# Kernel optimization log

Measured on AMD Instinct MI355X. Metric: run time of the kernel, lower is better.

The kernel has to match this reference:

```python
import jax, jax.numpy as jnp
import numpy as np

V_IN = 40962
V_POOL = 10242  # (V_IN + 6) // 4, icosahedral mesh
EPS = 1e-5


def _bn(x, g, b):
    # x: (B, V, C); per-sample BatchNorm1d over vertex axis (track_running_stats=False)
    m = jnp.mean(x, axis=1, keepdims=True)
    v = jnp.mean((x - m) ** 2, axis=1, keepdims=True)  # biased variance, as torch BN
    return (x - m) * jax.lax.rsqrt(v + EPS) * g + b


def _conv(x, idx, W, b):
    # x: (B, V, C); idx: (7*V,) neighbor order indices -> (B, V, 7*C) @ W + b
    B, V, C = x.shape
    g = x[:, idx, :].reshape(B, V, 7 * C)
    return jnp.einsum('bvk,ko->bvo', g, W) + b


def _lrelu(x):
    return jnp.where(x >= 0, x, 0.2 * x)


def setup_inputs() -> dict:
    key = jax.random.key(0)
    ks = jax.random.split(key, 4)
    C_in, C_out = 64, 128
    x = jax.random.normal(ks[0], (16, C_in, V_IN), dtype=jnp.float32)
    pool_neigh_orders = jax.random.randint(ks[1], (7 * V_POOL,), 0, V_IN, dtype=jnp.int64)
    neigh_orders = jax.random.randint(ks[2], (7 * V_POOL,), 0, V_POOL, dtype=jnp.int64)
    kw1, kw2 = jax.random.split(ks[3])
    W1 = jax.random.normal(kw1, (7 * C_in, C_out), dtype=jnp.float32) * 0.05
    W2 = jax.random.normal(kw2, (7 * C_out, C_out), dtype=jnp.float32) * 0.05
    return {
        'x': x,
        'pool_neigh_orders': pool_neigh_orders,
        'neigh_orders': neigh_orders,
        'W1': W1, 'b1': jnp.zeros((C_out,), jnp.float32),
        'g1': jnp.ones((C_out,), jnp.float32), 'beta1': jnp.zeros((C_out,), jnp.float32),
        'W2': W2, 'b2': jnp.zeros((C_out,), jnp.float32),
        'g2': jnp.ones((C_out,), jnp.float32), 'beta2': jnp.zeros((C_out,), jnp.float32),
    }


def reference(x, pool_neigh_orders, neigh_orders, W1, b1, g1, beta1, W2, b2, g2, beta2):
    # x: (B, C, V) -> work in (B, V, C)
    h = jnp.transpose(x, (0, 2, 1))
    B, _, C = h.shape
    # mean pool: (B, V_POOL, 7, C).mean over neighbors
    h = h[:, pool_neigh_orders, :].reshape(B, V_POOL, 7, C).mean(axis=2)
    h = _lrelu(_bn(_conv(h, neigh_orders, W1, b1), g1, beta1))
    h = _lrelu(_bn(_conv(h, neigh_orders, W2, b2), g2, beta2))
    return jnp.transpose(h, (0, 2, 1))  # (B, out_ch, V_POOL)
```

## Files before the change

kernel.cpp:

```cpp
#include <hip/hip_runtime.h>
#include <hip/hip_bf16.h>

#define NB 16
#define VIN 40962
#define VP 10242
#define EPSbn 1e-5f

typedef __attribute__((ext_vector_type(8))) short bf16x8;
typedef __attribute__((ext_vector_type(4))) float f32x4;
typedef unsigned short u16;

static constexpr size_t OFF_W2 = 0;
static constexpr size_t OFF_W1 = 458752;
static constexpr size_t OFF_Y1 = 688128;
static constexpr size_t OFF_ST = OFF_Y1 + (size_t)NB * VP * 128 * 4;
static constexpr size_t WS_NEED = OFF_ST + 8 * (size_t)NB * 128 * 4;
static constexpr size_t OFF_XT = WS_NEED;
static constexpr size_t WS_FAST = OFF_XT + (size_t)NB * VIN * 64 * 4;

__device__ __forceinline__ u16 f2bf(float f) {
    unsigned u; __builtin_memcpy(&u, &f, 4);
    u = u + 0x7FFF + ((u >> 16) & 1);
    return (u16)(u >> 16);
}
__device__ __forceinline__ float bf2f(u16 h) {
    unsigned u = ((unsigned)h) << 16; float f; __builtin_memcpy(&f, &u, 4); return f;
}
__device__ __forceinline__ ushort2 splitf(float f) {
    u16 h = f2bf(f);
    u16 l = f2bf(f - bf2f(h));
    ushort2 r; r.x = h; r.y = l; return r;
}

__global__ void k_wsplit(const float* __restrict__ W, u16* __restrict__ wts, int K)
{
    int idx = blockIdx.x * 256 + threadIdx.x;
    if (idx >= K * 128) return;
    int k = idx >> 7, o = idx & 127;
    ushort2 s = splitf(W[idx]);
    wts[(size_t)o * 2 * K + k]     = s.x;
    wts[(size_t)o * 2 * K + K + k] = s.y;
}

__global__ void k_transpose(const float* __restrict__ x, float* __restrict__ xT)
{
    __shared__ float t[64][65];
    const int b   = blockIdx.y;
    const int v0  = blockIdx.x * 64;
    const int tid = threadIdx.x;
    const int lc  = tid & 63;
    const int lw  = tid >> 6;
    const float* xb = x + (size_t)b * 64 * VIN;
#pragma unroll
    for (int u = 0; u < 16; ++u) {
        const int c = lw * 16 + u;
        const int v = v0 + lc;
        t[c][lc] = (v < VIN) ? xb[(size_t)c * VIN + v] : 0.f;
    }
    __syncthreads();
    float* xTb = xT + (size_t)b * VIN * 64;
#pragma unroll
    for (int u = 0; u < 16; ++u) {
        const int v = v0 + lw * 16 + u;
        if (v < VIN) xTb[(size_t)v * 64 + lc] = t[lc][lw * 16 + u];
    }
}

__global__ void k_pool_fast(const float* __restrict__ xT, const int* __restrict__ pidx,
                            u16* __restrict__ h0s)
{
    const int b  = blockIdx.y;
    const int vp = blockIdx.x * 4 + (threadIdx.x >> 6);
    const int c  = threadIdx.x & 63;
    if (vp >= VP) return;
    const float* xb = xT + (size_t)b * VIN * 64;
    float s = 0.f;
#pragma unroll
    for (int j = 0; j < 7; ++j) {
        const int id = pidx[vp * 7 + j];
        s += xb[(size_t)id * 64 + c];
    }
    s *= (1.f / 7.f);
    *(ushort2*)(h0s + ((size_t)b * VP + vp) * 128 + 2 * c) = splitf(s);
}

__global__ void k_pool_direct(const float* __restrict__ x, const int* __restrict__ pidx,
                              u16* __restrict__ h0s)
{
    const int b  = blockIdx.y;
    const int vp = blockIdx.x * 4 + (threadIdx.x >> 6);
    const int c  = threadIdx.x & 63;
    if (vp >= VP) return;
    const float* xb = x + (size_t)(b * 64) * VIN;
    float s = 0.f;
#pragma unroll
    for (int j = 0; j < 7; ++j) {
        const int id = pidx[vp * 7 + j];
        s += xb[(size_t)c * VIN + id];
    }
    s *= (1.f / 7.f);
    *(ushort2*)(h0s + ((size_t)b * VP + vp) * 128 + 2 * c) = splitf(s);
}

template<int CIN, bool TRANSOUT>
__global__ __launch_bounds__(256, 2)
void k_convm(const u16* __restrict__ src, const int* __restrict__ nidx,
             const u16* __restrict__ wts, const float* __restrict__ bias,
             float* __restrict__ y, float* __restrict__ gsum, float* __restrict__ gsq)
{
    constexpr int K = 7 * CIN;
    __shared__ float lt[TRANSOUT ? 128 : 1][129];

    const int tid = threadIdx.x;
    const int w   = tid >> 6;
    const int l   = tid & 63;
    const int lg  = l >> 4;
    const int lr  = l & 15;
    const int b   = blockIdx.y;
    const int vp0 = blockIdx.x * 128;
    const int r0  = vp0 + w * 32;

    const u16* srcb = src + (size_t)b * VP * (2 * CIN);
    const int vc0 = (r0 + lr      < VP) ? (r0 + lr)      : (VP - 1);
    const int vc1 = (r0 + 16 + lr < VP) ? (r0 + 16 + lr) : (VP - 1);

    const u16* bb[8];
#pragma unroll
    for (int ct = 0; ct < 8; ++ct) bb[ct] = wts + (size_t)(ct * 16 + lr) * (2 * K);

    f32x4 acc[2][8];
#pragma unroll
    for (int t = 0; t < 2; ++t)
#pragma unroll
        for (int ct = 0; ct < 8; ++ct) acc[t][ct] = (f32x4){0.f, 0.f, 0.f, 0.f};

    for (int j = 0; j < 7; ++j) {
        const int id0 = nidx[vc0 * 7 + j];
        const int id1 = nidx[vc1 * 7 + j];
        const u16* a0 = srcb + (size_t)id0 * (2 * CIN);
        const u16* a1 = srcb + (size_t)id1 * (2 * CIN);
#pragma unroll
        for (int ks = 0; ks < CIN / 32; ++ks) {
            const int ko = ks * 32 + lg * 8;
            bf16x8 p00 = *(const bf16x8*)(a0 + 2 * ko);
            bf16x8 p01 = *(const bf16x8*)(a0 + 2 * ko + 8);
            bf16x8 p10 = *(const bf16x8*)(a1 + 2 * ko);
            bf16x8 p11 = *(const bf16x8*)(a1 + 2 * ko + 8);
            bf16x8 ah0 = {p00[0], p00[2], p00[4], p00[6], p01[0], p01[2], p01[4], p01[6]};
            bf16x8 al0 = {p00[1], p00[3], p00[5], p00[7], p01[1], p01[3], p01[5], p01[7]};
            bf16x8 ah1 = {p10[0], p10[2], p10[4], p10[6], p11[0], p11[2], p11[4], p11[6]};
            bf16x8 al1 = {p10[1], p10[3], p10[5], p10[7], p11[1], p11[3], p11[5], p11[7]};
            const int kw = j * CIN + ko;
#pragma unroll
            for (int ct = 0; ct < 8; ++ct) {
                bf16x8 bh = *(const bf16x8*)(bb[ct] + kw);
                bf16x8 bl = *(const bf16x8*)(bb[ct] + kw + K);
                acc[0][ct] = __builtin_amdgcn_mfma_f32_16x16x32_bf16(ah0, bh, acc[0][ct], 0, 0, 0);
                acc[1][ct] = __builtin_amdgcn_mfma_f32_16x16x32_bf16(ah1, bh, acc[1][ct], 0, 0, 0);
                acc[0][ct] = __builtin_amdgcn_mfma_f32_16x16x32_bf16(al0, bh, acc[0][ct], 0, 0, 0);
                acc[1][ct] = __builtin_amdgcn_mfma_f32_16x16x32_bf16(al1, bh, acc[1][ct], 0, 0, 0);
                acc[0][ct] = __builtin_amdgcn_mfma_f32_16x16x32_bf16(ah0, bl, acc[0][ct], 0, 0, 0);
                acc[1][ct] = __builtin_amdgcn_mfma_f32_16x16x32_bf16(ah1, bl, acc[1][ct], 0, 0, 0);
            }
        }
    }

    float ssum[8], ssq[8];
#pragma unroll
    for (int ct = 0; ct < 8; ++ct) { ssum[ct] = 0.f; ssq[ct] = 0.f; }

#pragma unroll
    for (int ct = 0; ct < 8; ++ct) {
        const float bia = bias[ct * 16 + lr];
#pragma unroll
        for (int t = 0; t < 2; ++t) {
#pragma unroll
            for (int r = 0; r < 4; ++r) {
                const int row = r0 + t * 16 + lg * 4 + r;
                const float v = acc[t][ct][r] + bia;
                const bool ok = (row < VP);
                if constexpr (TRANSOUT) {
                    lt[w * 32 + t * 16 + lg * 4 + r][ct * 16 + lr] = v;
                } else {
                    if (ok) y[((size_t)b * VP + row) * 128 + ct * 16 + lr] = v;
                }
                if (ok) { ssum[ct] += v; ssq[ct] += v * v; }
            }
        }
    }
#pragma unroll
    for (int ct = 0; ct < 8; ++ct) {
        float s = ssum[ct], q = ssq[ct];
        s += __shfl_xor(s, 16, 64); s += __shfl_xor(s, 32, 64);
        q += __shfl_xor(q, 16, 64); q += __shfl_xor(q, 32, 64);
        if (l < 16) {
            atomicAdd(&gsum[b * 128 + ct * 16 + l], s);
            atomicAdd(&gsq [b * 128 + ct * 16 + l], q);
        }
    }
    if constexpr (TRANSOUT) {
        __syncthreads();
#pragma unroll
        for (int u = 0; u < 64; ++u) {
            const int idx = u * 256 + tid;
            const int ch = idx >> 7, vv = idx & 127;
            if (vp0 + vv < VP)
                y[((size_t)b * 128 + ch) * VP + vp0 + vv] = lt[vv][ch];
        }
    }
}

__global__ void k_finalize(const float* __restrict__ gsum, const float* __restrict__ gsq,
                           const float* __restrict__ gam, const float* __restrict__ bet,
                           float* __restrict__ scale, float* __restrict__ shift)
{
    const int i = blockIdx.x * 256 + threadIdx.x;
    if (i >= NB * 128) return;
    const int o = i & 127;
    const float m   = gsum[i] * (1.f / VP);
    const float var = gsq[i] * (1.f / VP) - m * m;
    const float sc  = gam[o] * rsqrtf(var + EPSbn);
    scale[i] = sc;
    shift[i] = fmaf(-m, sc, bet[o]);
}

__global__ void k_bn1(void* __restrict__ y1v, const float* __restrict__ sc1,
                      const float* __restrict__ sh1)
{
    const int b = blockIdx.y;
    float2* p = (float2*)y1v + (size_t)b * VP * 64;
    for (int e = blockIdx.x * 256 + threadIdx.x; e < VP * 64; e += gridDim.x * 256) {
        const int c = (e & 63) * 2;
        float2 f = p[e];
        const float2 sc = *(const float2*)(sc1 + b * 128 + c);
        const float2 sh = *(const float2*)(sh1 + b * 128 + c);
        float a0 = fmaf(f.x, sc.x, sh.x); a0 = (a0 >= 0.f) ? a0 : 0.2f * a0;
        float a1 = fmaf(f.y, sc.y, sh.y); a1 = (a1 >= 0.f) ? a1 : 0.2f * a1;
        const ushort2 s0 = splitf(a0), s1 = splitf(a1);
        ushort4 o; o.x = s0.x; o.y = s0.y; o.z = s1.x; o.w = s1.y;
        *(ushort4*)(p + e) = o;
    }
}

__global__ void k_bnout(float* __restrict__ out, const float* __restrict__ scale,
                        const float* __restrict__ shift)
{
    const int bo = blockIdx.x;
    const float sc = scale[bo], sh = shift[bo];
    float* p = out + (size_t)bo * VP;
    for (int v = threadIdx.x; v < VP; v += 256) {
        float xv = fmaf(p[v], sc, sh);
        p[v] = (xv >= 0.f) ? xv : 0.2f * xv;
    }
}

extern "C" void kernel_launch(void* const* d_in, const int* in_sizes, int n_in,
                              void* d_out, int out_size, void* d_ws, size_t ws_size,
                              hipStream_t stream)
{
    (void)in_sizes; (void)n_in; (void)out_size;
    const float* x   = (const float*)d_in[0];
    const int*   pidx= (const int*)d_in[1];
    const int*   nidx= (const int*)d_in[2];
    const float* W1  = (const float*)d_in[3];
    const float* b1  = (const float*)d_in[4];
    const float* g1  = (const float*)d_in[5];
    const float* be1 = (const float*)d_in[6];
    const float* W2  = (const float*)d_in[7];
    const float* b2  = (const float*)d_in[8];
    const float* g2  = (const float*)d_in[9];
    const float* be2 = (const float*)d_in[10];
    float* out = (float*)d_out;
    char*  ws  = (char*)d_ws;

    if (ws_size < WS_NEED) return;

    u16*   wts2 = (u16*)(ws + OFF_W2);
    u16*   wts1 = (u16*)(ws + OFF_W1);
    float* y1   = (float*)(ws + OFF_Y1);
    float* st   = (float*)(ws + OFF_ST);
    float* sum1 = st;          float* sq1 = st + 2048;
    float* sum2 = st + 4096;   float* sq2 = st + 6144;
    float* sc1  = st + 8192;   float* sh1 = st + 10240;
    float* sc2  = st + 12288;  float* sh2 = st + 14336;
    u16*   h0s  = (u16*)d_out;

    hipMemsetAsync(st, 0, 4 * 2048 * sizeof(float), stream);
    k_wsplit<<<224, 256, 0, stream>>>(W1, wts1, 448);
    k_wsplit<<<448, 256, 0, stream>>>(W2, wts2, 896);

    dim3 gpool((VP + 3) / 4, NB);
    if (ws_size >= WS_FAST) {
        float* xT = (float*)(ws + OFF_XT);
        dim3 gt((VIN + 63) / 64, NB);
        k_transpose<<<gt, 256, 0, stream>>>(x, xT);
        k_pool_fast<<<gpool, 256, 0, stream>>>(xT, pidx, h0s);
    } else {
        k_pool_direct<<<gpool, 256, 0, stream>>>(x, pidx, h0s);
    }

    dim3 gconv((VP + 127) / 128, NB);
    k_convm<64, false><<<gconv, 256, 0, stream>>>(h0s, nidx, wts1, b1, y1, sum1, sq1);
    k_finalize<<<8, 256, 0, stream>>>(sum1, sq1, g1, be1, sc1, sh1);
    k_bn1<<<dim3(160, NB), 256, 0, stream>>>(y1, sc1, sh1);
    k_convm<128, true><<<gconv, 256, 0, stream>>>((const u16*)y1, nidx, wts2, b2, out, sum2, sq2);
    k_finalize<<<8, 256, 0, stream>>>(sum2, sq2, g2, be2, sc2, sh2);
    k_bnout<<<2048, 256, 0, stream>>>(out, sc2, sh2);
}
```

Before: 1.033 ms.

## Pre-swizzle weights and activations for direct MFMA loads, remap grid per XCD

Weights are written in an MFMA-fragment-tiled layout, and activations store their hi and lo bf16 planes in separate halves of each row. Each lane can then load ready-made bf16x8 operands without shuffling elements. The conv kernel drops the LDS transpose and writes float4 columns directly, hoists the neighbor indices into registers, and raises the occupancy target to 4. Blocks are remapped so each XCD handles two batches, aiming at better L2 locality. The higher occupancy bound may force register spilling, and the grid mapping hardcodes 81 tiles and 8 XCDs.

```diff
diff --git a/kernel.cpp b/kernel.cpp
--- a/kernel.cpp
+++ b/kernel.cpp
@@ -37,9 +37,11 @@
     int idx = blockIdx.x * 256 + threadIdx.x;
     if (idx >= K * 128) return;
     int k = idx >> 7, o = idx & 127;
+    int ct = o >> 4, lr = o & 15, kt = k >> 5, lg = (k >> 3) & 3, e = k & 7;
+    size_t off = ((size_t)(ct * (K >> 5) + kt) << 9) + (lg * 16 + lr) * 8 + e;
     ushort2 s = splitf(W[idx]);
-    wts[(size_t)o * 2 * K + k]     = s.x;
-    wts[(size_t)o * 2 * K + K + k] = s.y;
+    wts[off]                  = s.x;
+    wts[off + (size_t)128 * K] = s.y;
 }
 
 __global__ void k_transpose(const float* __restrict__ x, float* __restrict__ xT)
@@ -81,7 +83,10 @@
         s += xb[(size_t)id * 64 + c];
     }
     s *= (1.f / 7.f);
-    *(ushort2*)(h0s + ((size_t)b * VP + vp) * 128 + 2 * c) = splitf(s);
+    u16* r = h0s + ((size_t)b * VP + vp) * 128;
+    ushort2 sp = splitf(s);
+    r[c]      = sp.x;
+    r[64 + c] = sp.y;
 }
 
 __global__ void k_pool_direct(const float* __restrict__ x, const int* __restrict__ pidx,
@@ -99,34 +104,47 @@
         s += xb[(size_t)c * VIN + id];
     }
     s *= (1.f / 7.f);
-    *(ushort2*)(h0s + ((size_t)b * VP + vp) * 128 + 2 * c) = splitf(s);
+    u16* r = h0s + ((size_t)b * VP + vp) * 128;
+    ushort2 sp = splitf(s);
+    r[c]      = sp.x;
+    r[64 + c] = sp.y;
 }
 
 template<int CIN, bool TRANSOUT>
-__global__ __launch_bounds__(256, 2)
+__global__ __launch_bounds__(256, 4)
 void k_convm(const u16* __restrict__ src, const int* __restrict__ nidx,
              const u16* __restrict__ wts, const float* __restrict__ bias,
              float* __restrict__ y, float* __restrict__ gsum, float* __restrict__ gsq)
 {
-    constexpr int K = 7 * CIN;
-    __shared__ float lt[TRANSOUT ? 128 : 1][129];
+    constexpr int K  = 7 * CIN;
+    constexpr int KT = K >> 5;
+    constexpr int PER = CIN >> 5;
 
     const int tid = threadIdx.x;
     const int w   = tid >> 6;
     const int l   = tid & 63;
     const int lg  = l >> 4;
     const int lr  = l & 15;
-    const int b   = blockIdx.y;
-    const int vp0 = blockIdx.x * 128;
-    const int r0  = vp0 + w * 32;
+
+    const int d    = blockIdx.x;
+    const int xcd  = d & 7;
+    const int s    = d >> 3;
+    const int hi   = (s >= 81) ? 1 : 0;
+    const int b    = xcd * 2 + hi;
+    const int tile = s - 81 * hi;
+    const int vp0  = tile * 128;
+    const int r0   = vp0 + w * 32;
 
     const u16* srcb = src + (size_t)b * VP * (2 * CIN);
     const int vc0 = (r0 + lr      < VP) ? (r0 + lr)      : (VP - 1);
     const int vc1 = (r0 + 16 + lr < VP) ? (r0 + 16 + lr) : (VP - 1);
 
-    const u16* bb[8];
-#pragma unroll
-    for (int ct = 0; ct < 8; ++ct) bb[ct] = wts + (size_t)(ct * 16 + lr) * (2 * K);
+    int id0[7], id1[7];
+#pragma unroll
+    for (int j = 0; j < 7; ++j) {
+        id0[j] = nidx[vc0 * 7 + j];
+        id1[j] = nidx[vc1 * 7 + j];
+    }
 
     f32x4 acc[2][8];
 #pragma unroll
@@ -134,27 +152,25 @@
 #pragma unroll
         for (int ct = 0; ct < 8; ++ct) acc[t][ct] = (f32x4){0.f, 0.f, 0.f, 0.f};
 
+    const u16* wl = wts + l * 8;
+
+#pragma unroll
     for (int j = 0; j < 7; ++j) {
-        const int id0 = nidx[vc0 * 7 + j];
-        const int id1 = nidx[vc1 * 7 + j];
-        const u16* a0 = srcb + (size_t)id0 * (2 * CIN);
-        const u16* a1 = srcb + (size_t)id1 * (2 * CIN);
-#pragma unroll
-        for (int ks = 0; ks < CIN / 32; ++ks) {
+        const u16* a0 = srcb + (size_t)id0[j] * (2 * CIN);
+        const u16* a1 = srcb + (size_t)id1[j] * (2 * CIN);
+#pragma unroll
+        for (int ks = 0; ks < PER; ++ks) {
             const int ko = ks * 32 + lg * 8;
-            bf16x8 p00 = *(const bf16x8*)(a0 + 2 * ko);
-            bf16x8 p01 = *(const bf16x8*)(a0 + 2 * ko + 8);
-            bf16x8 p10 = *(const bf16x8*)(a1 + 2 * ko);
-            bf16x8 p11 = *(const bf16x8*)(a1 + 2 * ko + 8);
-            bf16x8 ah0 = {p00[0], p00[2], p00[4], p00[6], p01[0], p01[2], p01[4], p01[6]};
-            bf16x8 al0 = {p00[1], p00[3], p00[5], p00[7], p01[1], p01[3], p01[5], p01[7]};
-            bf16x8 ah1 = {p10[0], p10[2], p10[4], p10[6], p11[0], p11[2], p11[4], p11[6]};
-            bf16x8 al1 = {p10[1], p10[3], p10[5], p10[7], p11[1], p11[3], p11[5], p11[7]};
-            const int kw = j * CIN + ko;
+            bf16x8 ah0 = *(const bf16x8*)(a0 + ko);
+            bf16x8 al0 = *(const bf16x8*)(a0 + CIN + ko);
+            bf16x8 ah1 = *(const bf16x8*)(a1 + ko);
+            bf16x8 al1 = *(const bf16x8*)(a1 + CIN + ko);
+            const int kt = j * PER + ks;
 #pragma unroll
             for (int ct = 0; ct < 8; ++ct) {
-                bf16x8 bh = *(const bf16x8*)(bb[ct] + kw);
-                bf16x8 bl = *(const bf16x8*)(bb[ct] + kw + K);
+                const u16* bp = wl + ((size_t)(ct * KT + kt) << 9);
+                bf16x8 bh = *(const bf16x8*)bp;
+                bf16x8 bl = *(const bf16x8*)(bp + (size_t)128 * K);
                 acc[0][ct] = __builtin_amdgcn_mfma_f32_16x16x32_bf16(ah0, bh, acc[0][ct], 0, 0, 0);
                 acc[1][ct] = __builtin_amdgcn_mfma_f32_16x16x32_bf16(ah1, bh, acc[1][ct], 0, 0, 0);
                 acc[0][ct] = __builtin_amdgcn_mfma_f32_16x16x32_bf16(al0, bh, acc[0][ct], 0, 0, 0);
@@ -174,38 +190,38 @@
         const float bia = bias[ct * 16 + lr];
 #pragma unroll
         for (int t = 0; t < 2; ++t) {
+            const int rbase = r0 + t * 16 + lg * 4;
 #pragma unroll
             for (int r = 0; r < 4; ++r) {
-                const int row = r0 + t * 16 + lg * 4 + r;
                 const float v = acc[t][ct][r] + bia;
-                const bool ok = (row < VP);
-                if constexpr (TRANSOUT) {
-                    lt[w * 32 + t * 16 + lg * 4 + r][ct * 16 + lr] = v;
+                acc[t][ct][r] = v;
+                if (rbase + r < VP) { ssum[ct] += v; ssq[ct] += v * v; }
+            }
+            if constexpr (TRANSOUT) {
+                float* q = y + ((size_t)b * 128 + ct * 16 + lr) * VP + rbase;
+                if (rbase + 3 < VP) {
+                    *(float4*)q = (float4){acc[t][ct][0], acc[t][ct][1], acc[t][ct][2], acc[t][ct][3]};
                 } else {
-                    if (ok) y[((size_t)b * VP + row) * 128 + ct * 16 + lr] = v;
+#pragma unroll
+                    for (int r = 0; r < 4; ++r)
+                        if (rbase + r < VP) q[r] = acc[t][ct][r];
                 }
-                if (ok) { ssum[ct] += v; ssq[ct] += v * v; }
+            } else {
+#pragma unroll
+                for (int r = 0; r < 4; ++r)
+                    if (rbase + r < VP)
+                        y[((size_t)b * VP + rbase + r) * 128 + ct * 16 + lr] = acc[t][ct][r];
             }
         }
     }
 #pragma unroll
     for (int ct = 0; ct < 8; ++ct) {
-        float s = ssum[ct], q = ssq[ct];
-        s += __shfl_xor(s, 16, 64); s += __shfl_xor(s, 32, 64);
-        q += __shfl_xor(q, 16, 64); q += __shfl_xor(q, 32, 64);
+        float su = ssum[ct], q = ssq[ct];
+        su += __shfl_xor(su, 16, 64); su += __shfl_xor(su, 32, 64);
+        q  += __shfl_xor(q,  16, 64); q  += __shfl_xor(q,  32, 64);
         if (l < 16) {
-            atomicAdd(&gsum[b * 128 + ct * 16 + l], s);
+            atomicAdd(&gsum[b * 128 + ct * 16 + l], su);
             atomicAdd(&gsq [b * 128 + ct * 16 + l], q);
-        }
-    }
-    if constexpr (TRANSOUT) {
-        __syncthreads();
-#pragma unroll
-        for (int u = 0; u < 64; ++u) {
-            const int idx = u * 256 + tid;
-            const int ch = idx >> 7, vv = idx & 127;
-            if (vp0 + vv < VP)
-                y[((size_t)b * 128 + ch) * VP + vp0 + vv] = lt[vv][ch];
         }
     }
 }
@@ -224,21 +240,25 @@
     shift[i] = fmaf(-m, sc, bet[o]);
 }
 
-__global__ void k_bn1(void* __restrict__ y1v, const float* __restrict__ sc1,
+__global__ void k_bn1(float* __restrict__ y1, const float* __restrict__ sc1,
                       const float* __restrict__ sh1)
 {
-    const int b = blockIdx.y;
-    float2* p = (float2*)y1v + (size_t)b * VP * 64;
-    for (int e = blockIdx.x * 256 + threadIdx.x; e < VP * 64; e += gridDim.x * 256) {
-        const int c = (e & 63) * 2;
-        float2 f = p[e];
-        const float2 sc = *(const float2*)(sc1 + b * 128 + c);
-        const float2 sh = *(const float2*)(sh1 + b * 128 + c);
-        float a0 = fmaf(f.x, sc.x, sh.x); a0 = (a0 >= 0.f) ? a0 : 0.2f * a0;
-        float a1 = fmaf(f.y, sc.y, sh.y); a1 = (a1 >= 0.f) ? a1 : 0.2f * a1;
+    const int wib = threadIdx.x >> 6;
+    const int l   = threadIdx.x & 63;
+    for (size_t row = (size_t)blockIdx.x * 4 + wib; row < (size_t)NB * VP;
+         row += (size_t)gridDim.x * 4) {
+        const int b = (int)(row / VP);
+        float2 v  = *(float2*)(y1 + row * 128 + 2 * l);
+        float2 sc = *(const float2*)(sc1 + b * 128 + 2 * l);
+        float2 sh = *(const float2*)(sh1 + b * 128 + 2 * l);
+        float a0 = fmaf(v.x, sc.x, sh.x); a0 = (a0 >= 0.f) ? a0 : 0.2f * a0;
+        float a1 = fmaf(v.y, sc.y, sh.y); a1 = (a1 >= 0.f) ? a1 : 0.2f * a1;
         const ushort2 s0 = splitf(a0), s1 = splitf(a1);
-        ushort4 o; o.x = s0.x; o.y = s0.y; o.z = s1.x; o.w = s1.y;
-        *(ushort4*)(p + e) = o;
+        u16* r = (u16*)(y1 + row * 128);
+        ushort2 h; h.x = s0.x; h.y = s1.x;
+        ushort2 lo; lo.x = s0.y; lo.y = s1.y;
+        *(ushort2*)(r + 2 * l)       = h;
+        *(ushort2*)(r + 128 + 2 * l) = lo;
     }
 }
 
@@ -299,11 +319,10 @@
         k_pool_direct<<<gpool, 256, 0, stream>>>(x, pidx, h0s);
     }
 
-    dim3 gconv((VP + 127) / 128, NB);
-    k_convm<64, false><<<gconv, 256, 0, stream>>>(h0s, nidx, wts1, b1, y1, sum1, sq1);
+    k_convm<64, false><<<1296, 256, 0, stream>>>(h0s, nidx, wts1, b1, y1, sum1, sq1);
     k_finalize<<<8, 256, 0, stream>>>(sum1, sq1, g1, be1, sc1, sh1);
-    k_bn1<<<dim3(160, NB), 256, 0, stream>>>(y1, sc1, sh1);
-    k_convm<128, true><<<gconv, 256, 0, stream>>>((const u16*)y1, nidx, wts2, b2, out, sum2, sq2);
+    k_bn1<<<2048, 256, 0, stream>>>(y1, sc1, sh1);
+    k_convm<128, true><<<1296, 256, 0, stream>>>((const u16*)y1, nidx, wts2, b2, out, sum2, sq2);
     k_finalize<<<8, 256, 0, stream>>>(sum2, sq2, g2, be2, sc2, sh2);
     k_bnout<<<2048, 256, 0, stream>>>(out, sc2, sh2);
 }
```

Measured after the change: 1.002 ms. -3.0%, faster.
